# Kernel optimization log

Hardware: AMD Instinct MI355X
Metric: run time of the kernel (lower is better)

Reference implementation:

```python
import jax, jax.numpy as jnp
import numpy as np

N_NODES = 10000
D_IN = 128
D_OUT = 128
N_EDGES = 640000


def setup_inputs() -> dict:
    key = jax.random.key(0)
    k_x, k_e, k_wl, k_wr, k_b = jax.random.split(key, 5)
    x = jax.random.normal(k_x, (N_NODES, D_IN), dtype=jnp.float32)
    edge_index = jax.random.randint(k_e, (2, N_EDGES), 0, N_NODES, dtype=jnp.int64)
    # SAGEConv params: lin_l (neighbor path, with bias), lin_r (root path, no bias)
    s_l = 1.0 / np.sqrt(D_IN)
    W_l = jax.random.uniform(k_wl, (D_OUT, D_IN), dtype=jnp.float32, minval=-s_l, maxval=s_l)
    b_l = jax.random.uniform(k_b, (D_OUT,), dtype=jnp.float32, minval=-s_l, maxval=s_l)
    W_r = jax.random.uniform(k_wr, (D_OUT, D_IN), dtype=jnp.float32, minval=-s_l, maxval=s_l)
    return {"x": x, "edge_index": edge_index, "W_l": W_l, "b_l": b_l, "W_r": W_r}


def reference(x, edge_index, W_l, b_l, W_r):
    x = x.astype(jnp.float32)
    src, dst = edge_index[0], edge_index[1]
    # gather source features, mean-aggregate into destination nodes
    msgs = x[src]                                   # [E, D_in] irregular gather
    agg_sum = jax.ops.segment_sum(msgs, dst, num_segments=N_NODES)  # [N, D_in]
    deg = jax.ops.segment_sum(jnp.ones((src.shape[0],), dtype=x.dtype), dst,
                              num_segments=N_NODES)                 # [N]
    agg = jnp.where(deg[:, None] > 0, agg_sum / jnp.maximum(deg, 1.0)[:, None], 0.0)
    # SAGEConv: lin_l(agg) + lin_r(x)
    y = agg @ W_l.T + b_l + x @ W_r.T               # [N, D_out]
    return x + y                                     # residual add
```

## Files before the change

### kernel.cpp

```cpp
#include <hip/hip_runtime.h>

#define N_NODES 10000
#define D 128
#define N_EDGES 640000
#define NB 256
#define HTHR 512
#define EPB (N_EDGES / NB)
#define SB 40
#define NPSB 250

typedef __attribute__((ext_vector_type(8))) short bf16x8;
typedef __attribute__((ext_vector_type(4))) float f32x4;
typedef __attribute__((ext_vector_type(8))) unsigned short us8;
typedef __attribute__((ext_vector_type(8))) float f32x8;

__device__ __forceinline__ unsigned short f2bf(float f) {
    union { float f; unsigned int i; } v;
    v.f = f;
    unsigned int b = v.i;
    unsigned int rounded = b + 0x7fffu + ((b >> 16) & 1u);
    return (unsigned short)(rounded >> 16);
}

__device__ __forceinline__ float bf2f(unsigned short u) {
    union { unsigned int i; float f; } v;
    v.i = ((unsigned int)u) << 16;
    return v.f;
}

__device__ __forceinline__ f32x8 bf2f8(us8 v) {
    f32x8 r;
#pragma unroll
    for (int t = 0; t < 8; ++t) r[t] = bf2f(v[t]);
    return r;
}


__global__ __launch_bounds__(HTHR) void hist_cast_kernel(const int* __restrict__ ei,
                                                         const float4* __restrict__ x4,
                                                         const float4* __restrict__ Wl4,
                                                         const float4* __restrict__ Wr4,
                                                         ushort4* __restrict__ xh4,
                                                         ushort4* __restrict__ Wlb4,
                                                         ushort4* __restrict__ Wrb4,
                                                         unsigned short* __restrict__ lrank,
                                                         unsigned short* __restrict__ cnt,
                                                         unsigned long long* __restrict__ flags) {
    __shared__ int h[N_NODES];
    const int tid = threadIdx.x;
    const int b = blockIdx.x;
    for (int n = tid; n < N_NODES; n += HTHR) h[n] = 0;
    if (b == 0 && tid < SB) flags[tid] = 0ULL;

    const int gid = b * HTHR + tid;
    for (int i = gid; i < N_NODES * D / 4; i += NB * HTHR) {
        float4 v = x4[i];
        ushort4 o;
        o.x = f2bf(v.x); o.y = f2bf(v.y); o.z = f2bf(v.z); o.w = f2bf(v.w);
        xh4[i] = o;
    }
    if (gid < D * D / 4) {
        float4 a = Wl4[gid], c = Wr4[gid];
        ushort4 oa, oc;
        oa.x = f2bf(a.x); oa.y = f2bf(a.y); oa.z = f2bf(a.z); oa.w = f2bf(a.w);
        oc.x = f2bf(c.x); oc.y = f2bf(c.y); oc.z = f2bf(c.z); oc.w = f2bf(c.w);
        Wlb4[gid] = oa;
        Wrb4[gid] = oc;
    }
    __syncthreads();

    const int base = b * EPB;
    for (int e = base + tid; e < base + EPB; e += HTHR) {
        int d = ei[N_EDGES + e];
        lrank[e] = (unsigned short)atomicAdd(&h[d], 1);
    }
    __syncthreads();
    unsigned short* c = cnt + (size_t)b * N_NODES;
    for (int n = tid; n < N_NODES; n += HTHR) c[n] = (unsigned short)h[n];
}


__global__ __launch_bounds__(256) void colscan_scan_kernel(unsigned short* __restrict__ cnt,
                                                           int* __restrict__ row_start,
                                                           unsigned long long* __restrict__ flags) {
    const int t = threadIdx.x;
    const int b = blockIdx.x;
    const int n = b * NPSB + t;
    __shared__ int sc[258];

    int deg = 0;
    if (t < NPSB) {
        int s = 0;
#pragma unroll 16
        for (int j = 0; j < NB; ++j) {
            int idx = j * N_NODES + n;
            int v = cnt[idx];
            cnt[idx] = (unsigned short)s;
            s += v;
        }
        deg = s;
    }
    sc[t] = deg;
    __syncthreads();
    for (int off = 1; off < 256; off <<= 1) {
        int v = (t >= off) ? sc[t - off] : 0;
        __syncthreads();
        sc[t] += v;
        __syncthreads();
    }
    const int total = sc[255];
    const int local_excl = sc[t] - deg;
    __syncthreads();

    if (b == 0) {
        if (t == 0) {
            __hip_atomic_store(&flags[0], (2ULL << 32) | (unsigned)total,
                               __ATOMIC_RELEASE, __HIP_MEMORY_SCOPE_AGENT);
            sc[256] = 0;
        }
    } else {
        if (t == 0) {
            __hip_atomic_store(&flags[b], (1ULL << 32) | (unsigned)total,
                               __ATOMIC_RELEASE, __HIP_MEMORY_SCOPE_AGENT);
        }
        if (t < 64) {
            const unsigned long long mask_b = (1ULL << b) - 1;
            int excl;
            for (;;) {
                unsigned long long f = (t < b)
                    ? __hip_atomic_load(&flags[t], __ATOMIC_ACQUIRE, __HIP_MEMORY_SCOPE_AGENT)
                    : (2ULL << 32);
                unsigned st = (unsigned)(f >> 32);
                unsigned long long ready = __ballot(st >= 1);
                if ((ready & mask_b) == mask_b) {
                    unsigned long long b2 = __ballot(st == 2) & mask_b;
                    int j = 63 - __builtin_clzll(b2 | 1ULL);
                    int v = (t >= j && t < b) ? (int)(unsigned)(f & 0xffffffffULL) : 0;
#pragma unroll
                    for (int off = 32; off > 0; off >>= 1) v += __shfl_down(v, off, 64);
                    excl = __shfl(v, 0, 64);
                    break;
                }
            }
            if (t == 0) {
                __hip_atomic_store(&flags[b], (2ULL << 32) | (unsigned)(excl + total),
                                   __ATOMIC_RELEASE, __HIP_MEMORY_SCOPE_AGENT);
                sc[256] = excl;
            }
        }
    }
    __syncthreads();
    if (t < NPSB) row_start[n] = sc[256] + local_excl;
    if (b == SB - 1 && t == 0) row_start[N_NODES] = N_EDGES;
}


__global__ __launch_bounds__(256) void scatter_kernel(const int* __restrict__ ei,
                                                      const int* __restrict__ row_start,
                                                      const unsigned short* __restrict__ cnt,
                                                      const unsigned short* __restrict__ lrank,
                                                      unsigned short* __restrict__ csr) {
    int i = blockIdx.x * 256 + threadIdx.x;
    if (i < N_EDGES) {
        int b = i / EPB;
        int s = ei[i];
        int d = ei[N_EDGES + i];
        int pos = row_start[d] + (int)cnt[(size_t)b * N_NODES + d] + (int)lrank[i];
        csr[pos] = (unsigned short)s;
    }
}


__global__ __launch_bounds__(256) void agg_lin_kernel(const float* __restrict__ x,
                                                      const unsigned short* __restrict__ xh,
                                                      const int* __restrict__ row_start,
                                                      const unsigned short* __restrict__ csr,
                                                      const unsigned short* __restrict__ Wlb,
                                                      const unsigned short* __restrict__ Wrb,
                                                      const float* __restrict__ bl,
                                                      float* __restrict__ out) {
    __shared__ __align__(16) unsigned short atile[16][136];
    const int tid = threadIdx.x;
    const int wave = tid >> 6;
    const int lane = tid & 63;
    const int slot = lane >> 4;
    const int lane16 = lane & 15;
    const int row0 = blockIdx.x * 16;
    const us8* xh8 = (const us8*)xh;

#pragma unroll
    for (int q = 0; q < 4; ++q) {
        const int node = row0 + wave * 4 + q;
        const int start = row_start[node];
        const int end = row_start[node + 1];
        f32x8 a0 = 0.f, a1 = 0.f, a2 = 0.f, a3 = 0.f;
        int j = start + slot;
        for (; j + 12 < end; j += 16) {
            int i0 = csr[j], i1 = csr[j + 4], i2 = csr[j + 8], i3 = csr[j + 12];
            us8 v0 = xh8[i0 * 16 + lane16];
            us8 v1 = xh8[i1 * 16 + lane16];
            us8 v2 = xh8[i2 * 16 + lane16];
            us8 v3 = xh8[i3 * 16 + lane16];
            a0 += bf2f8(v0); a1 += bf2f8(v1); a2 += bf2f8(v2); a3 += bf2f8(v3);
        }
        for (; j < end; j += 4) a0 += bf2f8(xh8[(int)csr[j] * 16 + lane16]);
        a0 = (a0 + a1) + (a2 + a3);
#pragma unroll
        for (int c = 0; c < 8; ++c) {
            float v = a0[c];
            v += __shfl_xor(v, 16, 64);
            v += __shfl_xor(v, 32, 64);
            a0[c] = v;
        }
        if (slot == 0) {
            int cntE = end - start;
            float inv = (cntE > 0) ? 1.0f / (float)cntE : 0.0f;
            us8 pack;
#pragma unroll
            for (int t = 0; t < 8; ++t) pack[t] = f2bf(a0[t] * inv);
            *(us8*)&atile[wave * 4 + q][lane16 * 8] = pack;
        }
    }
    __syncthreads();

    const int l15 = lane & 15;
    const int quad = lane >> 4;
    const int m = row0 + l15;
    const bf16x8* xrow = (const bf16x8*)(xh + (size_t)m * D) + quad;

    for (int ft = wave; ft < 8; ft += 4) {
        const int out0 = ft * 16;
        const int f = out0 + l15;
        const bf16x8* wlro = (const bf16x8*)(Wlb + (size_t)f * D) + quad;
        const bf16x8* wrro = (const bf16x8*)(Wrb + (size_t)f * D) + quad;

        f32x4 c = {0.f, 0.f, 0.f, 0.f};
#pragma unroll
        for (int kk = 0; kk < 4; ++kk) {
            bf16x8 afrag = *(const bf16x8*)&atile[l15][quad * 8 + kk * 32];
            c = __builtin_amdgcn_mfma_f32_16x16x32_bf16(afrag, wlro[kk * 4], c, 0, 0, 0);
            c = __builtin_amdgcn_mfma_f32_16x16x32_bf16(xrow[kk * 4], wrro[kk * 4], c, 0, 0, 0);
        }

        const float bias = bl[f];
#pragma unroll
        for (int r = 0; r < 4; ++r) {
            int row = row0 + quad * 4 + r;
            int idx = row * D + f;
            out[idx] = x[idx] + bias + c[r];
        }
    }
}

extern "C" void kernel_launch(void* const* d_in, const int* in_sizes, int n_in,
                              void* d_out, int out_size, void* d_ws, size_t ws_size,
                              hipStream_t stream) {
    const float* x  = (const float*)d_in[0];
    const int*   ei = (const int*)d_in[1];
    const float* Wl = (const float*)d_in[2];
    const float* bl = (const float*)d_in[3];
    const float* Wr = (const float*)d_in[4];
    float* out = (float*)d_out;

    unsigned long long* flags = (unsigned long long*)d_ws;
    int* row_start = (int*)(flags + 64);
    unsigned short* cnt   = (unsigned short*)(row_start + 10016);
    unsigned short* lrank = cnt + (size_t)NB * N_NODES;
    unsigned short* csr   = lrank + N_EDGES;
    unsigned short* xh    = csr + N_EDGES;
    unsigned short* Wlb   = xh + (size_t)N_NODES * D;
    unsigned short* Wrb   = Wlb + D * D;

    hist_cast_kernel<<<NB, HTHR, 0, stream>>>(ei, (const float4*)x, (const float4*)Wl,
                                              (const float4*)Wr, (ushort4*)xh,
                                              (ushort4*)Wlb, (ushort4*)Wrb,
                                              lrank, cnt, flags);
    colscan_scan_kernel<<<SB, 256, 0, stream>>>(cnt, row_start, flags);
    scatter_kernel<<<(N_EDGES + 255) / 256, 256, 0, stream>>>(ei, row_start, cnt, lrank, csr);
    agg_lin_kernel<<<N_NODES / 16, 256, 0, stream>>>(x, xh, row_start, csr,
                                                     Wlb, Wrb, bl, out);
}
```

Measured before the change: 122.5 us.

## Fuse scan, scatter and aggregation-linear into one persistent kernel with grid barriers

Merges the column scan, CSR scatter and aggregate+linear kernels into a single persistent launch of 500 blocks, separated by a software grid barrier built on an atomic counter in the flags workspace. The aim is to remove two kernel launch gaps and their drain/fill tails. In exchange it adds spin-wait barriers and depends on all 500 blocks being co-resident; launch bounds of 3 blocks per CU are meant to ensure that. The aggregation tiles are now looped over by a smaller grid, and the flags initialization grows to cover the barrier counter.

```diff
diff --git a/kernel.cpp b/kernel.cpp
--- a/kernel.cpp
+++ b/kernel.cpp
@@ -8,6 +8,7 @@
 #define EPB (N_EDGES / NB)
 #define SB 40
 #define NPSB 250
+#define NGRID 500
 
 typedef __attribute__((ext_vector_type(8))) short bf16x8;
 typedef __attribute__((ext_vector_type(4))) float f32x4;
@@ -33,6 +34,18 @@
 #pragma unroll
     for (int t = 0; t < 8; ++t) r[t] = bf2f(v[t]);
     return r;
+}
+
+__device__ __forceinline__ void gbar(unsigned int* bar, unsigned int target) {
+    __syncthreads();
+    if (threadIdx.x == 0) {
+        __builtin_amdgcn_fence(__ATOMIC_RELEASE, "agent");
+        __hip_atomic_fetch_add(bar, 1u, __ATOMIC_ACQ_REL, __HIP_MEMORY_SCOPE_AGENT);
+        while (__hip_atomic_load(bar, __ATOMIC_ACQUIRE, __HIP_MEMORY_SCOPE_AGENT) < target)
+            __builtin_amdgcn_s_sleep(2);
+        __builtin_amdgcn_fence(__ATOMIC_ACQUIRE, "agent");
+    }
+    __syncthreads();
 }
 
 
@@ -50,7 +63,7 @@
     const int tid = threadIdx.x;
     const int b = blockIdx.x;
     for (int n = tid; n < N_NODES; n += HTHR) h[n] = 0;
-    if (b == 0 && tid < SB) flags[tid] = 0ULL;
+    if (b == 0 && tid < 64) flags[tid] = 0ULL;
 
     const int gid = b * HTHR + tid;
     for (int i = gid; i < N_NODES * D / 4; i += NB * HTHR) {
@@ -80,175 +93,176 @@
 }
 
 
-__global__ __launch_bounds__(256) void colscan_scan_kernel(unsigned short* __restrict__ cnt,
+__global__ __launch_bounds__(256, 3) void sage_tail_kernel(const float* __restrict__ x,
+                                                           const int* __restrict__ ei,
+                                                           const unsigned short* __restrict__ xh,
+                                                           const unsigned short* __restrict__ Wlb,
+                                                           const unsigned short* __restrict__ Wrb,
+                                                           const float* __restrict__ bl,
+                                                           unsigned short* __restrict__ cnt,
+                                                           unsigned short* __restrict__ lrank,
+                                                           unsigned short* __restrict__ csr,
                                                            int* __restrict__ row_start,
-                                                           unsigned long long* __restrict__ flags) {
+                                                           unsigned long long* __restrict__ flags,
+                                                           float* __restrict__ out) {
+    __shared__ int sc[258];
+    __shared__ __align__(16) unsigned short atile[16][136];
+    unsigned int* bar = (unsigned int*)(flags + 48);
     const int t = threadIdx.x;
     const int b = blockIdx.x;
-    const int n = b * NPSB + t;
-    __shared__ int sc[258];
-
-    int deg = 0;
-    if (t < NPSB) {
-        int s = 0;
+
+    if (b < SB) {
+        const int n = b * NPSB + t;
+        int deg = 0;
+        if (t < NPSB) {
+            int s = 0;
 #pragma unroll 16
-        for (int j = 0; j < NB; ++j) {
-            int idx = j * N_NODES + n;
-            int v = cnt[idx];
-            cnt[idx] = (unsigned short)s;
-            s += v;
-        }
-        deg = s;
-    }
-    sc[t] = deg;
-    __syncthreads();
-    for (int off = 1; off < 256; off <<= 1) {
-        int v = (t >= off) ? sc[t - off] : 0;
-        __syncthreads();
-        sc[t] += v;
-        __syncthreads();
-    }
-    const int total = sc[255];
-    const int local_excl = sc[t] - deg;
-    __syncthreads();
-
-    if (b == 0) {
-        if (t == 0) {
-            __hip_atomic_store(&flags[0], (2ULL << 32) | (unsigned)total,
-                               __ATOMIC_RELEASE, __HIP_MEMORY_SCOPE_AGENT);
-            sc[256] = 0;
-        }
-    } else {
-        if (t == 0) {
-            __hip_atomic_store(&flags[b], (1ULL << 32) | (unsigned)total,
-                               __ATOMIC_RELEASE, __HIP_MEMORY_SCOPE_AGENT);
-        }
-        if (t < 64) {
-            const unsigned long long mask_b = (1ULL << b) - 1;
-            int excl;
-            for (;;) {
-                unsigned long long f = (t < b)
-                    ? __hip_atomic_load(&flags[t], __ATOMIC_ACQUIRE, __HIP_MEMORY_SCOPE_AGENT)
-                    : (2ULL << 32);
-                unsigned st = (unsigned)(f >> 32);
-                unsigned long long ready = __ballot(st >= 1);
-                if ((ready & mask_b) == mask_b) {
-                    unsigned long long b2 = __ballot(st == 2) & mask_b;
-                    int j = 63 - __builtin_clzll(b2 | 1ULL);
-                    int v = (t >= j && t < b) ? (int)(unsigned)(f & 0xffffffffULL) : 0;
-#pragma unroll
-                    for (int off = 32; off > 0; off >>= 1) v += __shfl_down(v, off, 64);
-                    excl = __shfl(v, 0, 64);
-                    break;
+            for (int j = 0; j < NB; ++j) {
+                int idx = j * N_NODES + n;
+                int v = cnt[idx];
+                cnt[idx] = (unsigned short)s;
+                s += v;
+            }
+            deg = s;
+        }
+        sc[t] = deg;
+        __syncthreads();
+        for (int off = 1; off < 256; off <<= 1) {
+            int v = (t >= off) ? sc[t - off] : 0;
+            __syncthreads();
+            sc[t] += v;
+            __syncthreads();
+        }
+        const int total = sc[255];
+        const int local_excl = sc[t] - deg;
+        __syncthreads();
+
+        if (b == 0) {
+            if (t == 0) {
+                __hip_atomic_store(&flags[0], (2ULL << 32) | (unsigned)total,
+                                   __ATOMIC_RELEASE, __HIP_MEMORY_SCOPE_AGENT);
+                sc[256] = 0;
+            }
+        } else {
+            if (t == 0) {
+                __hip_atomic_store(&flags[b], (1ULL << 32) | (unsigned)total,
+                                   __ATOMIC_RELEASE, __HIP_MEMORY_SCOPE_AGENT);
+            }
+            if (t < 64) {
+                const unsigned long long mask_b = (1ULL << b) - 1;
+                int excl;
+                for (;;) {
+                    unsigned long long f = (t < b)
+                        ? __hip_atomic_load(&flags[t], __ATOMIC_ACQUIRE, __HIP_MEMORY_SCOPE_AGENT)
+                        : (2ULL << 32);
+                    unsigned st = (unsigned)(f >> 32);
+                    unsigned long long ready = __ballot(st >= 1);
+                    if ((ready & mask_b) == mask_b) {
+                        unsigned long long b2 = __ballot(st == 2) & mask_b;
+                        int j = 63 - __builtin_clzll(b2 | 1ULL);
+                        int v = (t >= j && t < b) ? (int)(unsigned)(f & 0xffffffffULL) : 0;
+#pragma unroll
+                        for (int off = 32; off > 0; off >>= 1) v += __shfl_down(v, off, 64);
+                        excl = __shfl(v, 0, 64);
+                        break;
+                    }
                 }
-            }
-            if (t == 0) {
-                __hip_atomic_store(&flags[b], (2ULL << 32) | (unsigned)(excl + total),
-                                   __ATOMIC_RELEASE, __HIP_MEMORY_SCOPE_AGENT);
-                sc[256] = excl;
-            }
-        }
-    }
-    __syncthreads();
-    if (t < NPSB) row_start[n] = sc[256] + local_excl;
-    if (b == SB - 1 && t == 0) row_start[N_NODES] = N_EDGES;
-}
-
-
-__global__ __launch_bounds__(256) void scatter_kernel(const int* __restrict__ ei,
-                                                      const int* __restrict__ row_start,
-                                                      const unsigned short* __restrict__ cnt,
-                                                      const unsigned short* __restrict__ lrank,
-                                                      unsigned short* __restrict__ csr) {
-    int i = blockIdx.x * 256 + threadIdx.x;
-    if (i < N_EDGES) {
-        int b = i / EPB;
+                if (t == 0) {
+                    __hip_atomic_store(&flags[b], (2ULL << 32) | (unsigned)(excl + total),
+                                       __ATOMIC_RELEASE, __HIP_MEMORY_SCOPE_AGENT);
+                    sc[256] = excl;
+                }
+            }
+        }
+        __syncthreads();
+        if (t < NPSB) row_start[n] = sc[256] + local_excl;
+        if (b == SB - 1 && t == 0) row_start[N_NODES] = N_EDGES;
+    }
+
+    gbar(bar, 1 * NGRID);
+
+    for (int i = b * 256 + t; i < N_EDGES; i += NGRID * 256) {
+        int eb = i / EPB;
         int s = ei[i];
         int d = ei[N_EDGES + i];
-        int pos = row_start[d] + (int)cnt[(size_t)b * N_NODES + d] + (int)lrank[i];
+        int pos = row_start[d] + (int)cnt[(size_t)eb * N_NODES + d] + (int)lrank[i];
         csr[pos] = (unsigned short)s;
     }
-}
-
-
-__global__ __launch_bounds__(256) void agg_lin_kernel(const float* __restrict__ x,
-                                                      const unsigned short* __restrict__ xh,
-                                                      const int* __restrict__ row_start,
-                                                      const unsigned short* __restrict__ csr,
-                                                      const unsigned short* __restrict__ Wlb,
-                                                      const unsigned short* __restrict__ Wrb,
-                                                      const float* __restrict__ bl,
-                                                      float* __restrict__ out) {
-    __shared__ __align__(16) unsigned short atile[16][136];
-    const int tid = threadIdx.x;
-    const int wave = tid >> 6;
-    const int lane = tid & 63;
+
+    gbar(bar, 2 * NGRID);
+
+    const int wave = t >> 6;
+    const int lane = t & 63;
     const int slot = lane >> 4;
     const int lane16 = lane & 15;
-    const int row0 = blockIdx.x * 16;
-    const us8* xh8 = (const us8*)xh;
-
-#pragma unroll
-    for (int q = 0; q < 4; ++q) {
-        const int node = row0 + wave * 4 + q;
-        const int start = row_start[node];
-        const int end = row_start[node + 1];
-        f32x8 a0 = 0.f, a1 = 0.f, a2 = 0.f, a3 = 0.f;
-        int j = start + slot;
-        for (; j + 12 < end; j += 16) {
-            int i0 = csr[j], i1 = csr[j + 4], i2 = csr[j + 8], i3 = csr[j + 12];
-            us8 v0 = xh8[i0 * 16 + lane16];
-            us8 v1 = xh8[i1 * 16 + lane16];
-            us8 v2 = xh8[i2 * 16 + lane16];
-            us8 v3 = xh8[i3 * 16 + lane16];
-            a0 += bf2f8(v0); a1 += bf2f8(v1); a2 += bf2f8(v2); a3 += bf2f8(v3);
-        }
-        for (; j < end; j += 4) a0 += bf2f8(xh8[(int)csr[j] * 16 + lane16]);
-        a0 = (a0 + a1) + (a2 + a3);
-#pragma unroll
-        for (int c = 0; c < 8; ++c) {
-            float v = a0[c];
-            v += __shfl_xor(v, 16, 64);
-            v += __shfl_xor(v, 32, 64);
-            a0[c] = v;
-        }
-        if (slot == 0) {
-            int cntE = end - start;
-            float inv = (cntE > 0) ? 1.0f / (float)cntE : 0.0f;
-            us8 pack;
-#pragma unroll
-            for (int t = 0; t < 8; ++t) pack[t] = f2bf(a0[t] * inv);
-            *(us8*)&atile[wave * 4 + q][lane16 * 8] = pack;
-        }
-    }
-    __syncthreads();
-
     const int l15 = lane & 15;
     const int quad = lane >> 4;
-    const int m = row0 + l15;
-    const bf16x8* xrow = (const bf16x8*)(xh + (size_t)m * D) + quad;
-
-    for (int ft = wave; ft < 8; ft += 4) {
-        const int out0 = ft * 16;
-        const int f = out0 + l15;
-        const bf16x8* wlro = (const bf16x8*)(Wlb + (size_t)f * D) + quad;
-        const bf16x8* wrro = (const bf16x8*)(Wrb + (size_t)f * D) + quad;
-
-        f32x4 c = {0.f, 0.f, 0.f, 0.f};
-#pragma unroll
-        for (int kk = 0; kk < 4; ++kk) {
-            bf16x8 afrag = *(const bf16x8*)&atile[l15][quad * 8 + kk * 32];
-            c = __builtin_amdgcn_mfma_f32_16x16x32_bf16(afrag, wlro[kk * 4], c, 0, 0, 0);
-            c = __builtin_amdgcn_mfma_f32_16x16x32_bf16(xrow[kk * 4], wrro[kk * 4], c, 0, 0, 0);
-        }
-
-        const float bias = bl[f];
-#pragma unroll
-        for (int r = 0; r < 4; ++r) {
-            int row = row0 + quad * 4 + r;
-            int idx = row * D + f;
-            out[idx] = x[idx] + bias + c[r];
-        }
+    const us8* xh8 = (const us8*)xh;
+
+    for (int tile = b; tile < 625; tile += NGRID) {
+        const int row0 = tile * 16;
+
+#pragma unroll
+        for (int q = 0; q < 4; ++q) {
+            const int node = row0 + wave * 4 + q;
+            const int start = row_start[node];
+            const int end = row_start[node + 1];
+            f32x8 a0 = 0.f, a1 = 0.f, a2 = 0.f, a3 = 0.f;
+            int j = start + slot;
+            for (; j + 12 < end; j += 16) {
+                int i0 = csr[j], i1 = csr[j + 4], i2 = csr[j + 8], i3 = csr[j + 12];
+                us8 v0 = xh8[i0 * 16 + lane16];
+                us8 v1 = xh8[i1 * 16 + lane16];
+                us8 v2 = xh8[i2 * 16 + lane16];
+                us8 v3 = xh8[i3 * 16 + lane16];
+                a0 += bf2f8(v0); a1 += bf2f8(v1); a2 += bf2f8(v2); a3 += bf2f8(v3);
+            }
+            for (; j < end; j += 4) a0 += bf2f8(xh8[(int)csr[j] * 16 + lane16]);
+            a0 = (a0 + a1) + (a2 + a3);
+#pragma unroll
+            for (int c = 0; c < 8; ++c) {
+                float v = a0[c];
+                v += __shfl_xor(v, 16, 64);
+                v += __shfl_xor(v, 32, 64);
+                a0[c] = v;
+            }
+            if (slot == 0) {
+                int cntE = end - start;
+                float inv = (cntE > 0) ? 1.0f / (float)cntE : 0.0f;
+                us8 pack;
+#pragma unroll
+                for (int u = 0; u < 8; ++u) pack[u] = f2bf(a0[u] * inv);
+                *(us8*)&atile[wave * 4 + q][lane16 * 8] = pack;
+            }
+        }
+        __syncthreads();
+
+        const int m = row0 + l15;
+        const bf16x8* xrow = (const bf16x8*)(xh + (size_t)m * D) + quad;
+
+        for (int ft = wave; ft < 8; ft += 4) {
+            const int out0 = ft * 16;
+            const int f = out0 + l15;
+            const bf16x8* wlro = (const bf16x8*)(Wlb + (size_t)f * D) + quad;
+            const bf16x8* wrro = (const bf16x8*)(Wrb + (size_t)f * D) + quad;
+
+            f32x4 c = {0.f, 0.f, 0.f, 0.f};
+#pragma unroll
+            for (int kk = 0; kk < 4; ++kk) {
+                bf16x8 afrag = *(const bf16x8*)&atile[l15][quad * 8 + kk * 32];
+                c = __builtin_amdgcn_mfma_f32_16x16x32_bf16(afrag, wlro[kk * 4], c, 0, 0, 0);
+                c = __builtin_amdgcn_mfma_f32_16x16x32_bf16(xrow[kk * 4], wrro[kk * 4], c, 0, 0, 0);
+            }
+
+            const float bias = bl[f];
+#pragma unroll
+            for (int r = 0; r < 4; ++r) {
+                int row = row0 + quad * 4 + r;
+                int idx = row * D + f;
+                out[idx] = x[idx] + bias + c[r];
+            }
+        }
+        __syncthreads();
     }
 }
 
@@ -275,8 +289,6 @@
                                               (const float4*)Wr, (ushort4*)xh,
                                               (ushort4*)Wlb, (ushort4*)Wrb,
                                               lrank, cnt, flags);
-    colscan_scan_kernel<<<SB, 256, 0, stream>>>(cnt, row_start, flags);
-    scatter_kernel<<<(N_EDGES + 255) / 256, 256, 0, stream>>>(ei, row_start, cnt, lrank, csr);
-    agg_lin_kernel<<<N_NODES / 16, 256, 0, stream>>>(x, xh, row_start, csr,
-                                                     Wlb, Wrb, bl, out);
-}
+    sage_tail_kernel<<<NGRID, 256, 0, stream>>>(x, ei, xh, Wlb, Wrb, bl,
+                                                cnt, lrank, csr, row_start, flags, out);
+}
```

New measurement: 301.9 us. 2.46x slower.
